# Kernel tuning notes

Hardware: AMD Instinct MI355X
Metric: run time of the kernel (lower is better)

## Reference

```python
import jax, jax.numpy as jnp
import numpy as np


def setup_inputs() -> dict:
    key = jax.random.key(0)
    # image in roughly [-1, 1] as the normalization constants assume
    image = jnp.tanh(jax.random.normal(key, (1, 3, 256, 256), dtype=jnp.float32))
    return {"image": image, "kernel": 21}


def reference(image, kernel):
    """Faithful JAX port of WImage.wt_image(image, kernel, sigma=0.5, alpha=0.05).

    For each pixel and each RGB channel, sums exp(-(x_neigh - x_center)^2 / (2*sigma^2))
    over a k x k zero-padded window (nn.Unfold semantics), subtracts the self term (1),
    adds alpha * w to the image, then rescales with the analytic min/max.
    """
    sigma = 0.5
    alpha = 0.05
    k = int(kernel)
    p = k // 2
    n, c, H, W = image.shape

    # [1, c*k*k, H, W] -- zero padding exactly like nn.Unfold(kernel_size=(k,k), padding=p)
    patches = jax.lax.conv_general_dilated_patches(
        image, filter_shape=(k, k), window_strides=(1, 1),
        padding=((p, p), (p, p)))
    patches = patches.reshape(n, c, k * k, H, W)

    diff = patches - image[:, :, None, :, :]                 # neighbor - center
    g = jnp.exp(-(diff * diff) / (2.0 * sigma * sigma))      # gaussian affinity
    w = g.sum(axis=2) - 1.0                                  # drop self term -> [1, c, H, W]

    new_image = image + alpha * w

    no_of_neigh = k * k - 1
    mn = -1.0 + no_of_neigh * alpha * float(np.exp(-4.0 / (2.0 * sigma * sigma)))
    mx = 1.0 + no_of_neigh * alpha
    new_image = (new_image - mn) / (mx - mn)
    return new_image * 2.0 - 1.0
```

## Files before the change

### kernel.cpp

```cpp
#include <hip/hip_runtime.h>


#define NMOM 13
#define HH   256
#define WW   256
#define HRW  24

#define K2L  (-2.8853900817779268f)

template <int CTRL, int RMASK>
__device__ __forceinline__ float dpp_add(float v) {
    int s = __builtin_amdgcn_update_dpp(0, __builtin_bit_cast(int, v),
                                        CTRL, RMASK, 0xf, true);
    return v + __builtin_bit_cast(float, s);
}

__device__ __forceinline__ float wave_iscan(float v) {
    v = dpp_add<0x111, 0xf>(v);
    v = dpp_add<0x112, 0xf>(v);
    v = dpp_add<0x114, 0xf>(v);
    v = dpp_add<0x118, 0xf>(v);
    v = dpp_add<0x142, 0xa>(v);
    v = dpp_add<0x143, 0xc>(v);
    return v;
}

__global__ __launch_bounds__(256)
void wimage_reg(const float* __restrict__ img, float* __restrict__ out) {
    const int t    = threadIdx.x;
    const int lane = t & 63;
    const int w    = t >> 6;

    const int x0 = blockIdx.x * 32;
    const int yb = blockIdx.y * 16 + 4 * w;
    const int ch = blockIdx.z;
    const float* __restrict__ plane = img + ch * (HH * WW);

    const int  gx  = x0 - 10 + lane;
    const bool xok = (unsigned)gx < (unsigned)WW;

    float mu[HRW], n4[HRW];
    #pragma unroll
    for (int m = 0; m < HRW; ++m) {
        const int gy = yb - 10 + m;
        float n = 0.0f;
        if (xok && (unsigned)gy < (unsigned)HH) n = plane[gy * WW + gx];
        n4[m] = 4.0f * n;
        mu[m] = __builtin_amdgcn_exp2f(K2L * n * n);
    }

    float c[4], pw[4], acc[4];
    #pragma unroll
    for (int j = 0; j < 4; ++j) {
        c[j]  = (lane < 32) ? plane[(yb + j) * WW + x0 + lane] : 0.0f;
        pw[j] = 1.0f;
        acc[j] = 0.0f;
    }

    const float IKP1[NMOM] = {
        1.0f, 0.5f, 1.0f/3.0f, 0.25f, 0.2f, 1.0f/6.0f, 1.0f/7.0f, 0.125f,
        1.0f/9.0f, 0.1f, 1.0f/11.0f, 1.0f/12.0f, 1.0f/13.0f };

    #pragma unroll
    for (int k = 0; k < NMOM; ++k) {
        if (k > 0) {
            #pragma unroll
            for (int m = 0; m < HRW; ++m) mu[m] *= n4[m];
        }

        float sv0 = mu[0];
        #pragma unroll
        for (int m = 1; m < 21; ++m) sv0 += mu[m];
        float sv1 = sv0 - mu[0] + mu[21];
        float sv2 = sv1 - mu[1] + mu[22];
        float sv3 = sv2 - mu[2] + mu[23];
        if (k == 0) { sv0 -= 21.0f; sv1 -= 21.0f; sv2 -= 21.0f; sv3 -= 21.0f; }

        float sv[4] = { sv0, sv1, sv2, sv3 };
        #pragma unroll
        for (int j = 0; j < 4; ++j) {
            float p  = wave_iscan(sv[j]);
            float ph = __shfl(p, lane + 20);
            float pl = __shfl(p, lane - 1);
            float S  = ph - ((lane > 0) ? pl : 0.0f);
            acc[j] = fmaf(S, pw[j], acc[j]);
            pw[j] *= c[j] * IKP1[k];
        }
    }

    if (lane < 32) {
        const float alpha = 0.05f;
        const float mn    = -0.99261982218614470f;
        const float scale = 2.0f / (23.0f - mn);
        #pragma unroll
        for (int j = 0; j < 4; ++j) {
            const float cc  = c[j];
            const float e2c = __builtin_amdgcn_exp2f(K2L * cc * cc);
            const float tot = e2c * (acc[j] + 441.0f);
            out[ch * (HH * WW) + (yb + j) * WW + x0 + lane] =
                (cc + alpha * (tot - 1.0f) - mn) * scale - 1.0f;
        }
    }
}

extern "C" void kernel_launch(void* const* d_in, const int* in_sizes, int n_in,
                              void* d_out, int out_size, void* d_ws, size_t ws_size,
                              hipStream_t stream) {
    (void)in_sizes; (void)n_in; (void)out_size; (void)d_ws; (void)ws_size;
    const float* img = (const float*)d_in[0];
    float* out = (float*)d_out;

    dim3 grid(WW / 32, HH / 16, 3);
    wimage_reg<<<grid, dim3(256), 0, stream>>>(img, out);
}
```

Baseline: 12.77 us.

## Use 3 rows per wave, 128-thread blocks, 12 moments, direct bpermute shuffles

```diff
diff --git a/kernel.cpp b/kernel.cpp
--- a/kernel.cpp
+++ b/kernel.cpp
@@ -1,10 +1,12 @@
 #include <hip/hip_runtime.h>
 
 
-#define NMOM 13
+#define NMOM 12
 #define HH   256
 #define WW   256
-#define HRW  24
+#define RW   3
+#define HRW  (RW + 20)
+#define BROWS (2 * RW)
 
 #define K2L  (-2.8853900817779268f)
 
@@ -25,19 +27,22 @@
     return v;
 }
 
-__global__ __launch_bounds__(256)
+__global__ __launch_bounds__(128)
 void wimage_reg(const float* __restrict__ img, float* __restrict__ out) {
     const int t    = threadIdx.x;
     const int lane = t & 63;
     const int w    = t >> 6;
 
     const int x0 = blockIdx.x * 32;
-    const int yb = blockIdx.y * 16 + 4 * w;
+    const int yb = blockIdx.y * BROWS + RW * w;
     const int ch = blockIdx.z;
     const float* __restrict__ plane = img + ch * (HH * WW);
 
     const int  gx  = x0 - 10 + lane;
     const bool xok = (unsigned)gx < (unsigned)WW;
+
+    const int bp_hi = ((lane + 20) & 63) << 2;
+    const int bp_lo = ((lane - 1) & 63) << 2;
 
     float mu[HRW], n4[HRW];
     #pragma unroll
@@ -49,17 +54,18 @@
         mu[m] = __builtin_amdgcn_exp2f(K2L * n * n);
     }
 
-    float c[4], pw[4], acc[4];
+    float c[RW], pw[RW], acc[RW];
     #pragma unroll
-    for (int j = 0; j < 4; ++j) {
-        c[j]  = (lane < 32) ? plane[(yb + j) * WW + x0 + lane] : 0.0f;
+    for (int j = 0; j < RW; ++j) {
+        const int row = yb + j;
+        c[j]  = (lane < 32 && row < HH) ? plane[row * WW + x0 + lane] : 0.0f;
         pw[j] = 1.0f;
         acc[j] = 0.0f;
     }
 
     const float IKP1[NMOM] = {
         1.0f, 0.5f, 1.0f/3.0f, 0.25f, 0.2f, 1.0f/6.0f, 1.0f/7.0f, 0.125f,
-        1.0f/9.0f, 0.1f, 1.0f/11.0f, 1.0f/12.0f, 1.0f/13.0f };
+        1.0f/9.0f, 0.1f, 1.0f/11.0f, 1.0f/12.0f };
 
     #pragma unroll
     for (int k = 0; k < NMOM; ++k) {
@@ -73,15 +79,15 @@
         for (int m = 1; m < 21; ++m) sv0 += mu[m];
         float sv1 = sv0 - mu[0] + mu[21];
         float sv2 = sv1 - mu[1] + mu[22];
-        float sv3 = sv2 - mu[2] + mu[23];
-        if (k == 0) { sv0 -= 21.0f; sv1 -= 21.0f; sv2 -= 21.0f; sv3 -= 21.0f; }
+        if (k == 0) { sv0 -= 21.0f; sv1 -= 21.0f; sv2 -= 21.0f; }
 
-        float sv[4] = { sv0, sv1, sv2, sv3 };
+        float sv[RW] = { sv0, sv1, sv2 };
         #pragma unroll
-        for (int j = 0; j < 4; ++j) {
+        for (int j = 0; j < RW; ++j) {
             float p  = wave_iscan(sv[j]);
-            float ph = __shfl(p, lane + 20);
-            float pl = __shfl(p, lane - 1);
+            const int pi = __builtin_bit_cast(int, p);
+            float ph = __builtin_bit_cast(float, __builtin_amdgcn_ds_bpermute(bp_hi, pi));
+            float pl = __builtin_bit_cast(float, __builtin_amdgcn_ds_bpermute(bp_lo, pi));
             float S  = ph - ((lane > 0) ? pl : 0.0f);
             acc[j] = fmaf(S, pw[j], acc[j]);
             pw[j] *= c[j] * IKP1[k];
@@ -93,12 +99,15 @@
         const float mn    = -0.99261982218614470f;
         const float scale = 2.0f / (23.0f - mn);
         #pragma unroll
-        for (int j = 0; j < 4; ++j) {
-            const float cc  = c[j];
-            const float e2c = __builtin_amdgcn_exp2f(K2L * cc * cc);
-            const float tot = e2c * (acc[j] + 441.0f);
-            out[ch * (HH * WW) + (yb + j) * WW + x0 + lane] =
-                (cc + alpha * (tot - 1.0f) - mn) * scale - 1.0f;
+        for (int j = 0; j < RW; ++j) {
+            const int row = yb + j;
+            if (row < HH) {
+                const float cc  = c[j];
+                const float e2c = __builtin_amdgcn_exp2f(K2L * cc * cc);
+                const float tot = e2c * (acc[j] + 441.0f);
+                out[ch * (HH * WW) + row * WW + x0 + lane] =
+                    (cc + alpha * (tot - 1.0f) - mn) * scale - 1.0f;
+            }
         }
     }
 }
@@ -110,6 +119,6 @@
     const float* img = (const float*)d_in[0];
     float* out = (float*)d_out;
 
-    dim3 grid(WW / 32, HH / 16, 3);
-    wimage_reg<<<grid, dim3(256), 0, stream>>>(img, out);
+    dim3 grid(WW / 32, (HH + BROWS - 1) / BROWS, 3);
+    wimage_reg<<<grid, dim3(128), 0, stream>>>(img, out);
 }
```

New measurement: 12.99 us. No clear change (+1.8%).
